# Optimization experiments

Measured on AMD Instinct MI355X. Metric: run time of the kernel, lower is better.

## Reference

```python
import jax, jax.numpy as jnp
import numpy as np

B, L, K = 16384, 512, 4
N_ITERS = 5
EPS = 1e-08
NOISE_SCALE = 0.01


def setup_inputs() -> dict:
    key = jax.random.key(0)
    k1, k2, k3 = jax.random.split(key, 3)
    return {
        "windows": jax.random.normal(k1, (B, L), dtype=jnp.float32),
        "init_centers": jax.random.normal(k2, (K,), dtype=jnp.float32),
        "init_scales": jnp.ones((K,), dtype=jnp.float32),
        "init_weights": jnp.ones((K,), dtype=jnp.float32) / K,
        "prior_p_param": -jnp.ones((1,), dtype=jnp.float32),
        "weights_param": jnp.zeros((1, L), dtype=jnp.float32),
        "blend": jnp.zeros((1,), dtype=jnp.float32),
        "noise": jax.random.normal(k3, (B, K), dtype=jnp.float32),
    }


def _em(windows, init_centers, init_scales, init_weights,
        prior_p_param, weights_param, blend, noise):
    # windows: [B, L]
    data_mean = jnp.mean(windows, axis=-1, keepdims=True)          # [B, 1]
    data_std = jnp.std(windows, axis=-1, keepdims=True, ddof=1)    # [B, 1] (torch.std is unbiased)
    prior_var = jnp.var(windows, axis=-1, keepdims=True, ddof=1)   # [B, 1]

    # _initialize_parameters (noise passed in as standard normal, scaled here)
    mu = init_centers[None, :] * data_std + data_mean + noise * data_std * NOISE_SCALE  # [B, K]
    sigma = jnp.abs(init_scales)[None, :] * data_std                                    # [B, K]
    w = jnp.broadcast_to(init_weights[None, :], mu.shape)                               # [B, K]

    # _get_parameters
    weights = jnp.exp(weights_param)[..., None]   # [1, L, 1]
    blender = jax.nn.sigmoid(blend)               # [1]
    prior_p = jax.nn.sigmoid(prior_p_param)       # [1]

    g = None
    for _ in range(N_ITERS):
        # E-step: responsibilities via stable softmax over components
        log_w = jnp.log((w + EPS) / (sigma + EPS))[:, None, :]                 # [B, 1, K]
        z = (windows[..., None] - mu[:, None, :]) / (sigma[:, None, :] + EPS)  # [B, L, K]
        log_mix = -0.5 * z * z + log_w                                         # [B, L, K]
        g = jax.nn.softmax(log_mix, axis=-1)                                   # [B, L, K]

        # M-step
        wg = g * weights                                   # [B, L, K]
        sum_g = jnp.maximum(jnp.sum(wg, axis=-2), EPS)     # [B, K]
        w = sum_g + prior_p
        w = w / jnp.sum(w, axis=-1, keepdims=True)
        data_mu = jnp.sum(wg * windows[..., None], axis=-2) / sum_g            # [B, K]
        mu = data_mu * blender + data_mean * (1.0 - blender)                   # [B, K]
        diff = windows[..., None] - mu[:, None, :]                             # [B, L, K]
        data_var = jnp.sum(wg * diff * diff, axis=-2) / sum_g                  # [B, K]
        var = data_var * blender + prior_var * (1.0 - blender)
        sigma = jnp.sqrt(var + EPS)

    return g, w, mu, sigma


def reference(windows, init_centers, init_scales, init_weights,
              prior_p_param, weights_param, blend, noise):
    return _em(windows, init_centers, init_scales, init_weights,
               prior_p_param, weights_param, blend, noise)
```

## Files before the change

### kernel.cpp

```cpp
#include <hip/hip_runtime.h>
#include <math.h>


constexpr int Bn = 16384;
constexpr int Ln = 512;
constexpr int Kn = 4;
constexpr int NITER = 5;
constexpr float EPSf = 1e-8f;
constexpr float NOISEf = 0.01f;
constexpr float LOG2E = 1.4426950408889634f;

__device__ __forceinline__ float frcp(float v) { return __builtin_amdgcn_rcpf(v); }

template <int CTRL>
__device__ __forceinline__ float dpp_add(float v) {
    int t = __builtin_amdgcn_update_dpp(0, __float_as_int(v), CTRL, 0xF, 0xF, true);
    return v + __int_as_float(t);
}

__device__ __forceinline__ float wred_total(float v) {
    v = dpp_add<0x111>(v);
    v = dpp_add<0x112>(v);
    v = dpp_add<0x114>(v);
    v = dpp_add<0x118>(v);
    v = dpp_add<0x142>(v);
    v = dpp_add<0x143>(v);
    return __int_as_float(__builtin_amdgcn_readlane(__float_as_int(v), 63));
}

struct RowState {
    float x[8], xx[8], wl[8];
    float mu[4], w[4], inv_se[4], sig[4];
    float mean, prior_var, blender, omb, prior_p;
    float W0, W1, W2;
};

template <bool LAST>
__device__ __forceinline__ void em_iter(RowState& st, float* __restrict__ gout, int lane) {
    float A2[4], B2[4], C2[4];
#pragma unroll
    for (int k = 0; k < 4; ++k) {
        float is2 = st.inv_se[k] * st.inv_se[k];
        float lw2 = __log2f((st.w[k] + EPSf) * st.inv_se[k]);
        A2[k] = (-0.5f * LOG2E) * is2;
        B2[k] = (LOG2E * st.mu[k]) * is2;
        C2[k] = fmaf((-0.5f * LOG2E) * (st.mu[k] * st.mu[k]), is2, lw2);
    }

    float S0[3] = {0,0,0}, S1[3] = {0,0,0}, S2[3] = {0,0,0};
#pragma unroll
    for (int j = 0; j < 8; ++j) {
        float e[4];
        float esum = 0.f;
#pragma unroll
        for (int k = 0; k < 4; ++k) {
            float lm = fmaf(A2[k], st.xx[j], fmaf(B2[k], st.x[j], C2[k]));
            e[k] = __builtin_amdgcn_exp2f(lm);
            esum += e[k];
        }
        float inv = frcp(esum);
        float wls = st.wl[j] * inv;
        float wlsx = wls * st.x[j];
        float wlsxx = wls * st.xx[j];
#pragma unroll
        for (int k = 0; k < 3; ++k) {
            S0[k] = fmaf(e[k], wls,   S0[k]);
            S1[k] = fmaf(e[k], wlsx,  S1[k]);
            S2[k] = fmaf(e[k], wlsxx, S2[k]);
        }
        if (LAST) {
            float4 g4 = make_float4(e[0] * inv, e[1] * inv, e[2] * inv, e[3] * inv);
            *(float4*)(gout + (size_t)(lane + 64 * j) * 4) = g4;
        }
    }

    float T0[4], T1[4], T2[4];
#pragma unroll
    for (int k = 0; k < 3; ++k) {
        T0[k] = wred_total(S0[k]);
        T1[k] = wred_total(S1[k]);
        T2[k] = wred_total(S2[k]);
    }
    T0[3] = st.W0 - T0[0] - T0[1] - T0[2];
    T1[3] = st.W1 - T1[0] - T1[1] - T1[2];
    T2[3] = st.W2 - T2[0] - T2[1] - T2[2];

    float wn[4], wsum = 0.f;
#pragma unroll
    for (int k = 0; k < 4; ++k) {
        float sg = fmaxf(T0[k], EPSf);
        float rsg = frcp(sg);
        float dmu = T1[k] * rsg;
        float mun = fmaf(st.blender, dmu, st.omb * st.mean);
        float num = fmaf(mun * mun, T0[k], fmaf(-2.f * mun, T1[k], T2[k]));
        float dv = fmaxf(num * rsg, 0.f);
        float var = fmaf(st.blender, dv, st.omb * st.prior_var);
        float sgn = sqrtf(var + EPSf);
        st.mu[k] = mun;
        st.sig[k] = sgn;
        st.inv_se[k] = frcp(sgn + EPSf);
        wn[k] = sg + st.prior_p;
        wsum += wn[k];
    }
    float invws = frcp(wsum);
#pragma unroll
    for (int k = 0; k < 4; ++k) st.w[k] = wn[k] * invws;
}

__global__ __launch_bounds__(256, 4) void em_kernel(
    const float* __restrict__ windows,
    const float* __restrict__ centers,
    const float* __restrict__ scales,
    const float* __restrict__ iweights,
    const float* __restrict__ prior_p_param,
    const float* __restrict__ weights_param,
    const float* __restrict__ blend,
    const float* __restrict__ noise,
    float* __restrict__ out_g,
    float* __restrict__ out_w,
    float* __restrict__ out_mu,
    float* __restrict__ out_sigma)
{
    const int lane = threadIdx.x & 63;
    const int wv = threadIdx.x >> 6;
    const int b = blockIdx.x * 4 + wv;

    RowState st;
    const float* __restrict__ xr = windows + (size_t)b * Ln;
#pragma unroll
    for (int j = 0; j < 8; ++j) {
        float v = xr[lane + 64 * j];
        st.x[j] = v;
        st.xx[j] = v * v;
        st.wl[j] = __expf(weights_param[lane + 64 * j]);
    }

    float s = 0.f, ss = 0.f, w0 = 0.f, w1 = 0.f, w2 = 0.f;
#pragma unroll
    for (int j = 0; j < 8; ++j) {
        s += st.x[j];
        ss += st.xx[j];
        w0 += st.wl[j];
        w1 = fmaf(st.wl[j], st.x[j], w1);
        w2 = fmaf(st.wl[j], st.xx[j], w2);
    }
    s = wred_total(s);
    ss = wred_total(ss);
    st.W0 = wred_total(w0);
    st.W1 = wred_total(w1);
    st.W2 = wred_total(w2);

    st.mean = s * (1.0f / Ln);
    float var1 = fmaxf((ss - s * st.mean) * (1.0f / (Ln - 1)), 0.f);
    const float sd = sqrtf(var1);
    st.prior_var = var1;

    st.prior_p = 1.f / (1.f + __expf(-prior_p_param[0]));
    st.blender = 1.f / (1.f + __expf(-blend[0]));
    st.omb = 1.f - st.blender;

    const float4 nz = *(const float4*)(noise + (size_t)b * 4);
    const float nzv[4] = { nz.x, nz.y, nz.z, nz.w };

#pragma unroll
    for (int k = 0; k < 4; ++k) {
        st.mu[k] = fmaf(centers[k], sd, st.mean) + nzv[k] * sd * NOISEf;
        float sg0 = fabsf(scales[k]) * sd;
        st.sig[k] = sg0;
        st.w[k] = iweights[k];
        st.inv_se[k] = frcp(sg0 + EPSf);
    }

    float* gout = out_g + (size_t)b * Ln * Kn;
    for (int it = 0; it < NITER - 1; ++it)
        em_iter<false>(st, gout, lane);
    em_iter<true>(st, gout, lane);

    if (lane == 0) {
        *(float4*)(out_w     + (size_t)b * 4) = make_float4(st.w[0], st.w[1], st.w[2], st.w[3]);
        *(float4*)(out_mu    + (size_t)b * 4) = make_float4(st.mu[0], st.mu[1], st.mu[2], st.mu[3]);
        *(float4*)(out_sigma + (size_t)b * 4) = make_float4(st.sig[0], st.sig[1], st.sig[2], st.sig[3]);
    }
}

extern "C" void kernel_launch(void* const* d_in, const int* in_sizes, int n_in,
                              void* d_out, int out_size, void* d_ws, size_t ws_size,
                              hipStream_t stream) {
    const float* windows       = (const float*)d_in[0];
    const float* init_centers  = (const float*)d_in[1];
    const float* init_scales   = (const float*)d_in[2];
    const float* init_weights  = (const float*)d_in[3];
    const float* prior_p_param = (const float*)d_in[4];
    const float* weights_param = (const float*)d_in[5];
    const float* blend         = (const float*)d_in[6];
    const float* noise         = (const float*)d_in[7];

    float* out       = (float*)d_out;
    float* out_g     = out;
    float* out_w     = out_g + (size_t)Bn * Ln * Kn;
    float* out_mu    = out_w + (size_t)Bn * Kn;
    float* out_sigma = out_mu + (size_t)Bn * Kn;

    dim3 grid(Bn / 4);
    dim3 block(256);
    hipLaunchKernelGGL(em_kernel, grid, block, 0, stream,
                       windows, init_centers, init_scales, init_weights,
                       prior_p_param, weights_param, blend, noise,
                       out_g, out_w, out_mu, out_sigma);
}
```

Measured before the change: 213.0 us.

## Pack EM inner loop into paired FP32 math, reference component 4, batch DPP reductions

Rewrites the per-element E/M-step to use two-wide float vectors so the compiler can emit packed FP32 FMA/mul instructions. The softmax is re-expressed relative to component 3, so only three exp2 calls are needed per element and the fourth responsibility is just the reciprocal of the sum. Each lane now loads four contiguous floats (float4) instead of strided scalars, and the gamma output is written as two float4s per pair. Wave reductions are interleaved three at a time in inline DPP asm to hide DPP latency. The risks are overflow when component 3's term is tiny relative to the others, and hand-written asm nop/hazard handling.

```diff
diff --git a/kernel.cpp b/kernel.cpp
--- a/kernel.cpp
+++ b/kernel.cpp
@@ -10,26 +10,40 @@
 constexpr float NOISEf = 0.01f;
 constexpr float LOG2E = 1.4426950408889634f;
 
+typedef float v2f __attribute__((ext_vector_type(2)));
+
 __device__ __forceinline__ float frcp(float v) { return __builtin_amdgcn_rcpf(v); }
-
-template <int CTRL>
-__device__ __forceinline__ float dpp_add(float v) {
-    int t = __builtin_amdgcn_update_dpp(0, __float_as_int(v), CTRL, 0xF, 0xF, true);
-    return v + __int_as_float(t);
-}
-
-__device__ __forceinline__ float wred_total(float v) {
-    v = dpp_add<0x111>(v);
-    v = dpp_add<0x112>(v);
-    v = dpp_add<0x114>(v);
-    v = dpp_add<0x118>(v);
-    v = dpp_add<0x142>(v);
-    v = dpp_add<0x143>(v);
+__device__ __forceinline__ float fexp2(float v) { return __builtin_amdgcn_exp2f(v); }
+__device__ __forceinline__ v2f vfma(v2f a, v2f b, v2f c) {
+    return __builtin_elementwise_fma(a, b, c);
+}
+__device__ __forceinline__ v2f v2(float a, float b) { v2f r; r.x = a; r.y = b; return r; }
+__device__ __forceinline__ v2f v2u(float a) { v2f r; r.x = a; r.y = a; return r; }
+
+#define WRED3_STEP(ctrl) \
+    "v_add_f32_dpp %0, %0, %0 " ctrl " row_mask:0xf bank_mask:0xf bound_ctrl:0\n\t" \
+    "v_add_f32_dpp %1, %1, %1 " ctrl " row_mask:0xf bank_mask:0xf bound_ctrl:0\n\t" \
+    "v_add_f32_dpp %2, %2, %2 " ctrl " row_mask:0xf bank_mask:0xf bound_ctrl:0\n\t"
+
+__device__ __forceinline__ void wred3(float& a, float& b, float& c) {
+    asm volatile(
+        "s_nop 1\n\t"
+        WRED3_STEP("row_shr:1")
+        WRED3_STEP("row_shr:2")
+        WRED3_STEP("row_shr:4")
+        WRED3_STEP("row_shr:8")
+        WRED3_STEP("row_bcast:15")
+        WRED3_STEP("row_bcast:31")
+        "s_nop 1"
+        : "+v"(a), "+v"(b), "+v"(c));
+}
+
+__device__ __forceinline__ float lane63(float v) {
     return __int_as_float(__builtin_amdgcn_readlane(__float_as_int(v), 63));
 }
 
 struct RowState {
-    float x[8], xx[8], wl[8];
+    v2f x2[4], xx2[4], wl2[4];
     float mu[4], w[4], inv_se[4], sig[4];
     float mean, prior_var, blender, omb, prior_p;
     float W0, W1, W2;
@@ -37,49 +51,66 @@
 
 template <bool LAST>
 __device__ __forceinline__ void em_iter(RowState& st, float* __restrict__ gout, int lane) {
-    float A2[4], B2[4], C2[4];
+    float A[4], Bq[4], Cq[4];
 #pragma unroll
     for (int k = 0; k < 4; ++k) {
         float is2 = st.inv_se[k] * st.inv_se[k];
         float lw2 = __log2f((st.w[k] + EPSf) * st.inv_se[k]);
-        A2[k] = (-0.5f * LOG2E) * is2;
-        B2[k] = (LOG2E * st.mu[k]) * is2;
-        C2[k] = fmaf((-0.5f * LOG2E) * (st.mu[k] * st.mu[k]), is2, lw2);
-    }
-
-    float S0[3] = {0,0,0}, S1[3] = {0,0,0}, S2[3] = {0,0,0};
-#pragma unroll
-    for (int j = 0; j < 8; ++j) {
-        float e[4];
-        float esum = 0.f;
-#pragma unroll
-        for (int k = 0; k < 4; ++k) {
-            float lm = fmaf(A2[k], st.xx[j], fmaf(B2[k], st.x[j], C2[k]));
-            e[k] = __builtin_amdgcn_exp2f(lm);
-            esum += e[k];
+        A[k] = (-0.5f * LOG2E) * is2;
+        Bq[k] = (LOG2E * st.mu[k]) * is2;
+        Cq[k] = fmaf((-0.5f * LOG2E) * (st.mu[k] * st.mu[k]), is2, lw2);
+    }
+    v2f dA[3], dB[3], dC[3];
+#pragma unroll
+    for (int k = 0; k < 3; ++k) {
+        dA[k] = v2u(A[k] - A[3]);
+        dB[k] = v2u(Bq[k] - Bq[3]);
+        dC[k] = v2u(Cq[k] - Cq[3]);
+    }
+
+    v2f S0[3], S1[3], S2[3];
+#pragma unroll
+    for (int k = 0; k < 3; ++k) { S0[k] = v2u(0.f); S1[k] = v2u(0.f); S2[k] = v2u(0.f); }
+
+#pragma unroll
+    for (int p = 0; p < 4; ++p) {
+        v2f r[3];
+        v2f esum = v2u(1.f);
+#pragma unroll
+        for (int k = 0; k < 3; ++k) {
+            v2f lm = vfma(dA[k], st.xx2[p], vfma(dB[k], st.x2[p], dC[k]));
+            r[k] = v2(fexp2(lm.x), fexp2(lm.y));
+            esum += r[k];
         }
-        float inv = frcp(esum);
-        float wls = st.wl[j] * inv;
-        float wlsx = wls * st.x[j];
-        float wlsxx = wls * st.xx[j];
+        v2f inv = v2(frcp(esum.x), frcp(esum.y));
+        v2f wls = st.wl2[p] * inv;
+        v2f wlsx = wls * st.x2[p];
+        v2f wlsxx = wls * st.xx2[p];
 #pragma unroll
         for (int k = 0; k < 3; ++k) {
-            S0[k] = fmaf(e[k], wls,   S0[k]);
-            S1[k] = fmaf(e[k], wlsx,  S1[k]);
-            S2[k] = fmaf(e[k], wlsxx, S2[k]);
+            S0[k] = vfma(r[k], wls, S0[k]);
+            S1[k] = vfma(r[k], wlsx, S1[k]);
+            S2[k] = vfma(r[k], wlsxx, S2[k]);
         }
         if (LAST) {
-            float4 g4 = make_float4(e[0] * inv, e[1] * inv, e[2] * inv, e[3] * inv);
-            *(float4*)(gout + (size_t)(lane + 64 * j) * 4) = g4;
+            const int s0 = 256 * (p >> 1) + 4 * lane + 2 * (p & 1);
+            *(float4*)(gout + (size_t)s0 * 4) =
+                make_float4(r[0].x * inv.x, r[1].x * inv.x, r[2].x * inv.x, inv.x);
+            *(float4*)(gout + (size_t)(s0 + 1) * 4) =
+                make_float4(r[0].y * inv.y, r[1].y * inv.y, r[2].y * inv.y, inv.y);
         }
     }
 
     float T0[4], T1[4], T2[4];
 #pragma unroll
     for (int k = 0; k < 3; ++k) {
-        T0[k] = wred_total(S0[k]);
-        T1[k] = wred_total(S1[k]);
-        T2[k] = wred_total(S2[k]);
+        float t0 = S0[k].x + S0[k].y;
+        float t1 = S1[k].x + S1[k].y;
+        float t2 = S2[k].x + S2[k].y;
+        wred3(t0, t1, t2);
+        T0[k] = lane63(t0);
+        T1[k] = lane63(t1);
+        T2[k] = lane63(t2);
     }
     T0[3] = st.W0 - T0[0] - T0[1] - T0[2];
     T1[3] = st.W1 - T1[0] - T1[1] - T1[2];
@@ -127,28 +158,37 @@
 
     RowState st;
     const float* __restrict__ xr = windows + (size_t)b * Ln;
-#pragma unroll
-    for (int j = 0; j < 8; ++j) {
-        float v = xr[lane + 64 * j];
-        st.x[j] = v;
-        st.xx[j] = v * v;
-        st.wl[j] = __expf(weights_param[lane + 64 * j]);
-    }
-
-    float s = 0.f, ss = 0.f, w0 = 0.f, w1 = 0.f, w2 = 0.f;
-#pragma unroll
-    for (int j = 0; j < 8; ++j) {
-        s += st.x[j];
-        ss += st.xx[j];
-        w0 += st.wl[j];
-        w1 = fmaf(st.wl[j], st.x[j], w1);
-        w2 = fmaf(st.wl[j], st.xx[j], w2);
-    }
-    s = wred_total(s);
-    ss = wred_total(ss);
-    st.W0 = wred_total(w0);
-    st.W1 = wred_total(w1);
-    st.W2 = wred_total(w2);
+    const float4 q0 = *(const float4*)(xr + 4 * lane);
+    const float4 q1 = *(const float4*)(xr + 256 + 4 * lane);
+    st.x2[0] = v2(q0.x, q0.y); st.x2[1] = v2(q0.z, q0.w);
+    st.x2[2] = v2(q1.x, q1.y); st.x2[3] = v2(q1.z, q1.w);
+
+    const float4 e0 = *(const float4*)(weights_param + 4 * lane);
+    const float4 e1 = *(const float4*)(weights_param + 256 + 4 * lane);
+    st.wl2[0] = v2(__expf(e0.x), __expf(e0.y));
+    st.wl2[1] = v2(__expf(e0.z), __expf(e0.w));
+    st.wl2[2] = v2(__expf(e1.x), __expf(e1.y));
+    st.wl2[3] = v2(__expf(e1.z), __expf(e1.w));
+
+    v2f sv = v2u(0.f), ssv = v2u(0.f), w0v = v2u(0.f), w1v = v2u(0.f), w2v = v2u(0.f);
+#pragma unroll
+    for (int p = 0; p < 4; ++p) {
+        st.xx2[p] = st.x2[p] * st.x2[p];
+        sv += st.x2[p];
+        ssv += st.xx2[p];
+        w0v += st.wl2[p];
+        w1v = vfma(st.wl2[p], st.x2[p], w1v);
+        w2v = vfma(st.wl2[p], st.xx2[p], w2v);
+    }
+    float s = sv.x + sv.y, ss = ssv.x + ssv.y, w0 = w0v.x + w0v.y;
+    float w1 = w1v.x + w1v.y, w2 = w2v.x + w2v.y, junk = 0.f;
+    wred3(s, ss, w0);
+    wred3(w1, w2, junk);
+    s = lane63(s);
+    ss = lane63(ss);
+    st.W0 = lane63(w0);
+    st.W1 = lane63(w1);
+    st.W2 = lane63(w2);
 
     st.mean = s * (1.0f / Ln);
     float var1 = fmaxf((ss - s * st.mean) * (1.0f / (Ln - 1)), 0.f);
```

After: 203.1 us. -4.7%, faster.

## Spread per-component state across lanes and normalize softmax against the last component

Applied to the files above, without the earlier changes.

Each lane now holds the EM parameters of a single component (lane&3), and the E-step coefficients are broadcast through swizzles and readlanes. The softmax is taken relative to component 3, which saves one exp per element. Wave reductions are batched three at a time in inline DPP assembly, and window loads become float4 with a matching permuted element order. The aim is to cut the scalar per-k work and the transcendental count. The trade-off is reliance on hand-written DPP asm with its hazard nops, plus possible precision loss from dividing by exp of component 3.

```diff
diff --git a/kernel.cpp b/kernel.cpp
--- a/kernel.cpp
+++ b/kernel.cpp
@@ -11,100 +11,110 @@
 constexpr float LOG2E = 1.4426950408889634f;
 
 __device__ __forceinline__ float frcp(float v) { return __builtin_amdgcn_rcpf(v); }
-
-template <int CTRL>
-__device__ __forceinline__ float dpp_add(float v) {
-    int t = __builtin_amdgcn_update_dpp(0, __float_as_int(v), CTRL, 0xF, 0xF, true);
-    return v + __int_as_float(t);
-}
-
-__device__ __forceinline__ float wred_total(float v) {
-    v = dpp_add<0x111>(v);
-    v = dpp_add<0x112>(v);
-    v = dpp_add<0x114>(v);
-    v = dpp_add<0x118>(v);
-    v = dpp_add<0x142>(v);
-    v = dpp_add<0x143>(v);
-    return __int_as_float(__builtin_amdgcn_readlane(__float_as_int(v), 63));
+__device__ __forceinline__ float fexp2(float v) { return __builtin_amdgcn_exp2f(v); }
+
+template <int IMM>
+__device__ __forceinline__ float swz(float v) {
+    return __int_as_float(__builtin_amdgcn_ds_swizzle(__float_as_int(v), IMM));
+}
+__device__ __forceinline__ float rlane(float v, int l) {
+    return __int_as_float(__builtin_amdgcn_readlane(__float_as_int(v), l));
+}
+
+#define WRED3_STEP(ctrl) \
+    "v_add_f32_dpp %0, %0, %0 " ctrl " row_mask:0xf bank_mask:0xf bound_ctrl:0\n\t" \
+    "v_add_f32_dpp %1, %1, %1 " ctrl " row_mask:0xf bank_mask:0xf bound_ctrl:0\n\t" \
+    "v_add_f32_dpp %2, %2, %2 " ctrl " row_mask:0xf bank_mask:0xf bound_ctrl:0\n\t"
+
+__device__ __forceinline__ void wred3(float& a, float& b, float& c) {
+    asm volatile(
+        "s_nop 1\n\t"
+        WRED3_STEP("row_shr:1")
+        WRED3_STEP("row_shr:2")
+        WRED3_STEP("row_shr:4")
+        WRED3_STEP("row_shr:8")
+        WRED3_STEP("row_bcast:15")
+        WRED3_STEP("row_bcast:31")
+        "s_nop 1"
+        : "+v"(a), "+v"(b), "+v"(c));
 }
 
 struct RowState {
     float x[8], xx[8], wl[8];
-    float mu[4], w[4], inv_se[4], sig[4];
-    float mean, prior_var, blender, omb, prior_p;
+    float muk, wk, invsek, sigk;
+    float mean, prior_var, blender, prior_p;
+    float bm, bv;
     float W0, W1, W2;
 };
 
 template <bool LAST>
-__device__ __forceinline__ void em_iter(RowState& st, float* __restrict__ gout, int lane) {
-    float A2[4], B2[4], C2[4];
-#pragma unroll
-    for (int k = 0; k < 4; ++k) {
-        float is2 = st.inv_se[k] * st.inv_se[k];
-        float lw2 = __log2f((st.w[k] + EPSf) * st.inv_se[k]);
-        A2[k] = (-0.5f * LOG2E) * is2;
-        B2[k] = (LOG2E * st.mu[k]) * is2;
-        C2[k] = fmaf((-0.5f * LOG2E) * (st.mu[k] * st.mu[k]), is2, lw2);
-    }
-
-    float S0[3] = {0,0,0}, S1[3] = {0,0,0}, S2[3] = {0,0,0};
+__device__ __forceinline__ void em_iter(RowState& st, float* __restrict__ gout,
+                                        int lane, int kk) {
+    float is2 = st.invsek * st.invsek;
+    float lw2 = __log2f((st.wk + EPSf) * st.invsek);
+    float Ak = (-0.5f * LOG2E) * is2;
+    float Bk = (LOG2E * st.muk) * is2;
+    float Ck = fmaf((-0.5f * LOG2E) * (st.muk * st.muk), is2, lw2);
+    float dAl = Ak - swz<0x7F>(Ak);
+    float dBl = Bk - swz<0x7F>(Bk);
+    float dCl = Ck - swz<0x7F>(Ck);
+    float a0 = rlane(dAl, 0), a1 = rlane(dAl, 1), a2 = rlane(dAl, 2);
+    float b0 = rlane(dBl, 0), b1 = rlane(dBl, 1), b2 = rlane(dBl, 2);
+    float c0 = rlane(dCl, 0), c1 = rlane(dCl, 1), c2 = rlane(dCl, 2);
+
+    float S00 = 0, S01 = 0, S02 = 0;
+    float S10 = 0, S11 = 0, S12 = 0;
+    float S20 = 0, S21 = 0, S22 = 0;
 #pragma unroll
     for (int j = 0; j < 8; ++j) {
-        float e[4];
-        float esum = 0.f;
-#pragma unroll
-        for (int k = 0; k < 4; ++k) {
-            float lm = fmaf(A2[k], st.xx[j], fmaf(B2[k], st.x[j], C2[k]));
-            e[k] = __builtin_amdgcn_exp2f(lm);
-            esum += e[k];
-        }
+        float lm0 = fmaf(a0, st.xx[j], fmaf(b0, st.x[j], c0));
+        float lm1 = fmaf(a1, st.xx[j], fmaf(b1, st.x[j], c1));
+        float lm2 = fmaf(a2, st.xx[j], fmaf(b2, st.x[j], c2));
+        float r0 = fexp2(lm0);
+        float r1 = fexp2(lm1);
+        float r2 = fexp2(lm2);
+        float esum = 1.f + r0 + r1 + r2;
         float inv = frcp(esum);
         float wls = st.wl[j] * inv;
         float wlsx = wls * st.x[j];
         float wlsxx = wls * st.xx[j];
-#pragma unroll
-        for (int k = 0; k < 3; ++k) {
-            S0[k] = fmaf(e[k], wls,   S0[k]);
-            S1[k] = fmaf(e[k], wlsx,  S1[k]);
-            S2[k] = fmaf(e[k], wlsxx, S2[k]);
-        }
+        S00 = fmaf(r0, wls, S00); S10 = fmaf(r0, wlsx, S10); S20 = fmaf(r0, wlsxx, S20);
+        S01 = fmaf(r1, wls, S01); S11 = fmaf(r1, wlsx, S11); S21 = fmaf(r1, wlsxx, S21);
+        S02 = fmaf(r2, wls, S02); S12 = fmaf(r2, wlsx, S12); S22 = fmaf(r2, wlsxx, S22);
         if (LAST) {
-            float4 g4 = make_float4(e[0] * inv, e[1] * inv, e[2] * inv, e[3] * inv);
-            *(float4*)(gout + (size_t)(lane + 64 * j) * 4) = g4;
+            const int idx = (j < 4) ? (4 * lane + j) : (256 + 4 * lane + (j - 4));
+            *(float4*)(gout + (size_t)idx * 4) =
+                make_float4(r0 * inv, r1 * inv, r2 * inv, inv);
         }
     }
 
-    float T0[4], T1[4], T2[4];
-#pragma unroll
-    for (int k = 0; k < 3; ++k) {
-        T0[k] = wred_total(S0[k]);
-        T1[k] = wred_total(S1[k]);
-        T2[k] = wred_total(S2[k]);
-    }
-    T0[3] = st.W0 - T0[0] - T0[1] - T0[2];
-    T1[3] = st.W1 - T1[0] - T1[1] - T1[2];
-    T2[3] = st.W2 - T2[0] - T2[1] - T2[2];
-
-    float wn[4], wsum = 0.f;
-#pragma unroll
-    for (int k = 0; k < 4; ++k) {
-        float sg = fmaxf(T0[k], EPSf);
-        float rsg = frcp(sg);
-        float dmu = T1[k] * rsg;
-        float mun = fmaf(st.blender, dmu, st.omb * st.mean);
-        float num = fmaf(mun * mun, T0[k], fmaf(-2.f * mun, T1[k], T2[k]));
-        float dv = fmaxf(num * rsg, 0.f);
-        float var = fmaf(st.blender, dv, st.omb * st.prior_var);
-        float sgn = sqrtf(var + EPSf);
-        st.mu[k] = mun;
-        st.sig[k] = sgn;
-        st.inv_se[k] = frcp(sgn + EPSf);
-        wn[k] = sg + st.prior_p;
-        wsum += wn[k];
-    }
-    float invws = frcp(wsum);
-#pragma unroll
-    for (int k = 0; k < 4; ++k) st.w[k] = wn[k] * invws;
+    wred3(S00, S10, S20);
+    wred3(S01, S11, S21);
+    wred3(S02, S12, S22);
+    float s00 = rlane(S00, 63), s10 = rlane(S10, 63), s20 = rlane(S20, 63);
+    float s01 = rlane(S01, 63), s11 = rlane(S11, 63), s21 = rlane(S21, 63);
+    float s02 = rlane(S02, 63), s12 = rlane(S12, 63), s22 = rlane(S22, 63);
+    float d0 = st.W0 - s00 - s01 - s02;
+    float d1 = st.W1 - s10 - s11 - s12;
+    float d2 = st.W2 - s20 - s21 - s22;
+    float vT0 = (kk == 0) ? s00 : (kk == 1) ? s01 : (kk == 2) ? s02 : d0;
+    float vT1 = (kk == 0) ? s10 : (kk == 1) ? s11 : (kk == 2) ? s12 : d1;
+    float vT2 = (kk == 0) ? s20 : (kk == 1) ? s21 : (kk == 2) ? s22 : d2;
+
+    float sg = fmaxf(vT0, EPSf);
+    float rsg = frcp(sg);
+    float mun = fmaf(st.blender, vT1 * rsg, st.bm);
+    float num = fmaf(mun * mun, vT0, fmaf(-2.f * mun, vT1, vT2));
+    float dv = fmaxf(num * rsg, 0.f);
+    float var = fmaf(st.blender, dv, st.bv);
+    float sgn = sqrtf(var + EPSf);
+    st.muk = mun;
+    st.sigk = sgn;
+    st.invsek = frcp(sgn + EPSf);
+    float wn = sg + st.prior_p;
+    float ws = wn + swz<0x041F>(wn);
+    ws = ws + swz<0x081F>(ws);
+    st.wk = wn * frcp(ws);
 }
 
 __global__ __launch_bounds__(256, 4) void em_kernel(
@@ -122,33 +132,41 @@
     float* __restrict__ out_sigma)
 {
     const int lane = threadIdx.x & 63;
-    const int wv = threadIdx.x >> 6;
-    const int b = blockIdx.x * 4 + wv;
+    const int kk = lane & 3;
+    const int b = blockIdx.x * 4 + (threadIdx.x >> 6);
 
     RowState st;
     const float* __restrict__ xr = windows + (size_t)b * Ln;
-#pragma unroll
-    for (int j = 0; j < 8; ++j) {
-        float v = xr[lane + 64 * j];
-        st.x[j] = v;
-        st.xx[j] = v * v;
-        st.wl[j] = __expf(weights_param[lane + 64 * j]);
-    }
+    const float4 q0 = *(const float4*)(xr + 4 * lane);
+    const float4 q1 = *(const float4*)(xr + 256 + 4 * lane);
+    st.x[0] = q0.x; st.x[1] = q0.y; st.x[2] = q0.z; st.x[3] = q0.w;
+    st.x[4] = q1.x; st.x[5] = q1.y; st.x[6] = q1.z; st.x[7] = q1.w;
+
+    const float4 e0 = *(const float4*)(weights_param + 4 * lane);
+    const float4 e1 = *(const float4*)(weights_param + 256 + 4 * lane);
+    st.wl[0] = __expf(e0.x); st.wl[1] = __expf(e0.y);
+    st.wl[2] = __expf(e0.z); st.wl[3] = __expf(e0.w);
+    st.wl[4] = __expf(e1.x); st.wl[5] = __expf(e1.y);
+    st.wl[6] = __expf(e1.z); st.wl[7] = __expf(e1.w);
 
     float s = 0.f, ss = 0.f, w0 = 0.f, w1 = 0.f, w2 = 0.f;
 #pragma unroll
     for (int j = 0; j < 8; ++j) {
+        st.xx[j] = st.x[j] * st.x[j];
         s += st.x[j];
         ss += st.xx[j];
         w0 += st.wl[j];
         w1 = fmaf(st.wl[j], st.x[j], w1);
         w2 = fmaf(st.wl[j], st.xx[j], w2);
     }
-    s = wred_total(s);
-    ss = wred_total(ss);
-    st.W0 = wred_total(w0);
-    st.W1 = wred_total(w1);
-    st.W2 = wred_total(w2);
+    float junk = 0.f;
+    wred3(s, ss, w0);
+    wred3(w1, w2, junk);
+    s = rlane(s, 63);
+    ss = rlane(ss, 63);
+    st.W0 = rlane(w0, 63);
+    st.W1 = rlane(w1, 63);
+    st.W2 = rlane(w2, 63);
 
     st.mean = s * (1.0f / Ln);
     float var1 = fmaxf((ss - s * st.mean) * (1.0f / (Ln - 1)), 0.f);
@@ -157,29 +175,25 @@
 
     st.prior_p = 1.f / (1.f + __expf(-prior_p_param[0]));
     st.blender = 1.f / (1.f + __expf(-blend[0]));
-    st.omb = 1.f - st.blender;
-
-    const float4 nz = *(const float4*)(noise + (size_t)b * 4);
-    const float nzv[4] = { nz.x, nz.y, nz.z, nz.w };
-
-#pragma unroll
-    for (int k = 0; k < 4; ++k) {
-        st.mu[k] = fmaf(centers[k], sd, st.mean) + nzv[k] * sd * NOISEf;
-        float sg0 = fabsf(scales[k]) * sd;
-        st.sig[k] = sg0;
-        st.w[k] = iweights[k];
-        st.inv_se[k] = frcp(sg0 + EPSf);
-    }
+    const float omb = 1.f - st.blender;
+    st.bm = omb * st.mean;
+    st.bv = omb * st.prior_var;
+
+    st.muk = fmaf(centers[kk], sd, st.mean) + noise[(size_t)b * 4 + kk] * sd * NOISEf;
+    float sg0 = fabsf(scales[kk]) * sd;
+    st.sigk = sg0;
+    st.wk = iweights[kk];
+    st.invsek = frcp(sg0 + EPSf);
 
     float* gout = out_g + (size_t)b * Ln * Kn;
     for (int it = 0; it < NITER - 1; ++it)
-        em_iter<false>(st, gout, lane);
-    em_iter<true>(st, gout, lane);
-
-    if (lane == 0) {
-        *(float4*)(out_w     + (size_t)b * 4) = make_float4(st.w[0], st.w[1], st.w[2], st.w[3]);
-        *(float4*)(out_mu    + (size_t)b * 4) = make_float4(st.mu[0], st.mu[1], st.mu[2], st.mu[3]);
-        *(float4*)(out_sigma + (size_t)b * 4) = make_float4(st.sig[0], st.sig[1], st.sig[2], st.sig[3]);
+        em_iter<false>(st, gout, lane, kk);
+    em_iter<true>(st, gout, lane, kk);
+
+    if (lane < 4) {
+        out_w[(size_t)b * 4 + lane]     = st.wk;
+        out_mu[(size_t)b * 4 + lane]    = st.muk;
+        out_sigma[(size_t)b * 4 + lane] = st.sigk;
     }
 }
 
```

Measured after the change: 198.0 us. -7.1%, faster.
